# Performance work log

Hardware: AMD Instinct MI355X
Metric: run time of the kernel (lower is better)

## Reference

```python
import jax, jax.numpy as jnp
import numpy as np

B, S, D = 8, 2048, 512
FF = 2048
E = 8

def setup_inputs() -> dict:
    key = jax.random.key(0)
    ks = jax.random.split(key, 7)
    s = 1.0 / np.sqrt(D)
    sf = 1.0 / np.sqrt(FF)
    return {
        "x":  jax.random.normal(ks[0], (B, S, D), dtype=jnp.float32),
        "Wg": jax.random.uniform(ks[1], (D, E), jnp.float32, -s, s),
        "bg": jax.random.uniform(ks[2], (E,), jnp.float32, -s, s),
        "W1": jax.random.uniform(ks[3], (E, D, FF), jnp.float32, -s, s),
        "b1": jax.random.uniform(ks[4], (E, FF), jnp.float32, -s, s),
        "W2": jax.random.uniform(ks[5], (E, FF, D), jnp.float32, -sf, sf),
        "b2": jax.random.uniform(ks[6], (E, D), jnp.float32, -sf, sf),
    }

def reference(x, Wg, bg, W1, b1, W2, b2):
    b, s, d = x.shape
    xf = x.reshape(-1, d)                      # [T, D]
    logits = xf @ Wg + bg                      # [T, E]
    probs = jax.nn.softmax(logits, axis=-1)
    pmax = jnp.max(probs, axis=-1)             # [T]
    routes = jnp.argmax(probs, axis=-1)        # [T] int
    xs = xf * pmax[:, None]                    # scale tokens by router prob
    # per-expert FFN over all tokens, select the routed expert's output
    out_tok = jnp.zeros_like(xf)
    for e in range(E):
        h = jax.nn.relu(xs @ W1[e] + b1[e])    # [T, FF]
        y = h @ W2[e] + b2[e]                  # [T, D]
        out_tok = jnp.where((routes == e)[:, None], y, out_tok)
    # torch.cat of per-expert nonzero-index gathers == tokens stably sorted by expert id
    order = jnp.argsort(routes)                # jnp.argsort is stable
    return out_tok[order].reshape(b, s, d)
```

## Files before the change

### kernel.cpp

```cpp
#include <hip/hip_runtime.h>
#include <hip/hip_bf16.h>

constexpr int TTOK  = 16384;
constexpr int DDIM  = 512;
constexpr int FFDIM = 2048;
constexpr int NEXP  = 8;
constexpr int GB_TOK = 16;
constexpr int NGB    = TTOK / GB_TOK;
constexpr int MAXTILES = TTOK / 128 + NEXP;
constexpr int TRW1_BLOCKS = 4096;
constexpr int TRW2_XBLK   = 256;

typedef __attribute__((ext_vector_type(8))) short short8_t;
typedef __attribute__((ext_vector_type(4))) float f32x4_t;

__device__ __forceinline__ unsigned short f2bf(float f) {
    union { float f; unsigned u; } v; v.f = f;
    return (unsigned short)((v.u + 0x7fffu + ((v.u >> 16) & 1u)) >> 16);
}

__device__ __forceinline__ void gl_lds16(const void* g, void* l) {
    __builtin_amdgcn_global_load_lds(
        (const __attribute__((address_space(1))) void*)g,
        (__attribute__((address_space(3))) void*)l,
        16, 0, 0);
}

__device__ __forceinline__ void tr_tile(const float* __restrict__ src,
                                        unsigned short* __restrict__ dst,
                                        int R, int C, int tileId, float* lds) {
    int tilesC = C / 32;
    int c0 = (tileId % tilesC) * 32;
    int r0 = (tileId / tilesC) * 64;
    int t = threadIdx.x;
    int lr = t >> 3;
    int ls = t & 7;
    #pragma unroll
    for (int rb = 0; rb < 2; rb++) {
        int row = rb * 32 + lr;
        float4 v = *(const float4*)(src + (size_t)(r0 + row) * C + c0 + 4 * ls);
        int p4 = (4 * ls) ^ (8 * ((row >> 3) & 3));
        *(float4*)(lds + row * 36 + p4) = v;
    }
    __syncthreads();
    int c = t >> 3;
    int b = t & 7;
    union { short8_t v; unsigned short s[8]; } o;
    #pragma unroll
    for (int j = 0; j < 8; j++) {
        int r = 8 * b + j;
        int p = c ^ (8 * ((r >> 3) & 3));
        o.s[j] = f2bf(lds[r * 36 + p]);
    }
    *(short8_t*)(dst + (size_t)(c0 + c) * R + r0 + 8 * b) = o.v;
}

__global__ __launch_bounds__(256) void gate_kernel(const float* __restrict__ x,
                                                   const float* __restrict__ Wg,
                                                   const float* __restrict__ bg,
                                                   int* __restrict__ route,
                                                   float* __restrict__ pmax,
                                                   int* __restrict__ blockCounts) {
    int tid = threadIdx.x;
    __shared__ int cnt[NEXP];
    __shared__ float bgs[NEXP];
    int gb = blockIdx.x;
    if (tid < NEXP) { cnt[tid] = 0; bgs[tid] = bg[tid]; }
    __syncthreads();
    int wave = tid >> 6, lane = tid & 63;
    float w[8][8];
    #pragma unroll
    for (int jj = 0; jj < 8; jj++) {
        float4 a = *(const float4*)(Wg + (size_t)(lane * 8 + jj) * NEXP);
        float4 b = *(const float4*)(Wg + (size_t)(lane * 8 + jj) * NEXP + 4);
        w[jj][0] = a.x; w[jj][1] = a.y; w[jj][2] = a.z; w[jj][3] = a.w;
        w[jj][4] = b.x; w[jj][5] = b.y; w[jj][6] = b.z; w[jj][7] = b.w;
    }
    int tbase = gb * GB_TOK + wave * 4;
    for (int it = 0; it < 4; it++) {
        int t = tbase + it;
        float4 xa = *(const float4*)(x + (size_t)t * DDIM + lane * 8);
        float4 xb = *(const float4*)(x + (size_t)t * DDIM + lane * 8 + 4);
        float xs[8] = {xa.x, xa.y, xa.z, xa.w, xb.x, xb.y, xb.z, xb.w};
        double acc[NEXP];
        #pragma unroll
        for (int e = 0; e < NEXP; e++) acc[e] = 0.0;
        #pragma unroll
        for (int jj = 0; jj < 8; jj++) {
            double xv = (double)xs[jj];
            #pragma unroll
            for (int e = 0; e < NEXP; e++) acc[e] += xv * (double)w[jj][e];
        }
        #pragma unroll
        for (int off = 32; off > 0; off >>= 1) {
            #pragma unroll
            for (int e = 0; e < NEXP; e++) acc[e] += __shfl_down(acc[e], off);
        }
        if (lane == 0) {
            double l[NEXP];
            #pragma unroll
            for (int e = 0; e < NEXP; e++) l[e] = acc[e] + (double)bgs[e];
            int r = 0; double lm = l[0];
            #pragma unroll
            for (int e = 1; e < NEXP; e++) if (l[e] > lm) { lm = l[e]; r = e; }
            float s = 0.0f;
            #pragma unroll
            for (int e = 0; e < NEXP; e++) s += __expf((float)(l[e] - lm));
            route[t] = r;
            pmax[t] = 1.0f / s;
            atomicAdd(&cnt[r], 1);
        }
    }
    __syncthreads();
    if (tid < NEXP) blockCounts[gb * NEXP + tid] = cnt[tid];
}

__global__ __launch_bounds__(256) void scatter_kernel(const float* __restrict__ x,
                                                      const int* __restrict__ route,
                                                      const float* __restrict__ pmax,
                                                      const int* __restrict__ blockCounts,
                                                      unsigned short* __restrict__ Xs,
                                                      int* __restrict__ segPrefix,
                                                      int* __restrict__ tilePrefix,
                                                      const float* __restrict__ W1,
                                                      unsigned short* __restrict__ W1T) {
    int tid = threadIdx.x;
    if (blockIdx.x >= NGB) {
        __shared__ __align__(16) float tlds[64 * 36];
        int id = blockIdx.x - NGB;
        int e = id >> 9;
        int tile = id & 511;
        tr_tile(W1 + (size_t)e * DDIM * FFDIM, W1T + (size_t)e * DDIM * FFDIM,
                DDIM, FFDIM, tile, tlds);
        return;
    }
    int bb = blockIdx.x;
    int wave = tid >> 6, lane = tid & 63;

    int tot[NEXP], pre[NEXP];
    #pragma unroll
    for (int e = 0; e < NEXP; e++) { tot[e] = 0; pre[e] = 0; }
    for (int b = tid; b < NGB; b += 256) {
        #pragma unroll
        for (int e = 0; e < NEXP; e++) {
            int c = blockCounts[b * NEXP + e];
            tot[e] += c;
            if (b < bb) pre[e] += c;
        }
    }
    #pragma unroll
    for (int off = 32; off > 0; off >>= 1) {
        #pragma unroll
        for (int e = 0; e < NEXP; e++) {
            tot[e] += __shfl_down(tot[e], off);
            pre[e] += __shfl_down(pre[e], off);
        }
    }
    __shared__ int stot[4][NEXP], spre[4][NEXP];
    __shared__ int boff[NEXP];
    if (lane == 0) {
        #pragma unroll
        for (int e = 0; e < NEXP; e++) { stot[wave][e] = tot[e]; spre[wave][e] = pre[e]; }
    }
    __syncthreads();
    if (tid == 0) {
        int T[NEXP], P[NEXP];
        #pragma unroll
        for (int e = 0; e < NEXP; e++) {
            T[e] = stot[0][e] + stot[1][e] + stot[2][e] + stot[3][e];
            P[e] = spre[0][e] + spre[1][e] + spre[2][e] + spre[3][e];
        }
        int s = 0;
        #pragma unroll
        for (int e = 0; e < NEXP; e++) { boff[e] = s + P[e]; s += T[e]; }
        if (bb == 0) {
            int ss = 0, tp = 0;
            segPrefix[0] = 0; tilePrefix[0] = 0;
            #pragma unroll
            for (int e = 0; e < NEXP; e++) {
                ss += T[e]; tp += (T[e] + 127) >> 7;
                segPrefix[e + 1] = ss; tilePrefix[e + 1] = tp;
            }
        }
    }
    __syncthreads();

    __shared__ int dstL[GB_TOK];
    __shared__ float pmL[GB_TOK];
    if (tid < GB_TOK) {
        int t = bb * GB_TOK + tid;
        int r = route[t];
        unsigned long long ltmask = (tid == 0) ? 0ull : ((~0ull) >> (64 - tid));
        int rank = 0;
        #pragma unroll
        for (int e = 0; e < NEXP; e++) {
            unsigned long long m = __ballot(r == e);
            if (r == e) rank = __popcll(m & ltmask);
        }
        dstL[tid] = boff[r] + rank;
        pmL[tid] = pmax[t];
    }
    __syncthreads();
    for (int rr = 0; rr < 4; rr++) {
        int rowl = wave * 4 + rr;
        int t = bb * GB_TOK + rowl;
        float pm = pmL[rowl];
        const float4* xr = (const float4*)(x + (size_t)t * DDIM) + lane * 2;
        float4 a = xr[0], b = xr[1];
        union { short8_t v; unsigned short s[8]; } o;
        o.s[0] = f2bf(a.x * pm); o.s[1] = f2bf(a.y * pm);
        o.s[2] = f2bf(a.z * pm); o.s[3] = f2bf(a.w * pm);
        o.s[4] = f2bf(b.x * pm); o.s[5] = f2bf(b.y * pm);
        o.s[6] = f2bf(b.z * pm); o.s[7] = f2bf(b.w * pm);
        *(short8_t*)(Xs + (size_t)dstL[rowl] * DDIM + lane * 8) = o.v;
    }
}

__global__ __launch_bounds__(256) void gemm1_fused(const unsigned short* __restrict__ A,
                                                   const unsigned short* __restrict__ Bt,
                                                   const float* __restrict__ bias,
                                                   unsigned short* __restrict__ C,
                                                   const int* __restrict__ segPrefix,
                                                   const int* __restrict__ tilePrefix,
                                                   const float* __restrict__ W2,
                                                   unsigned short* __restrict__ W2T) {
    constexpr int K = DDIM, N = FFDIM;
    __shared__ __align__(16) unsigned short SMEM[16384];

    if (blockIdx.x >= MAXTILES) {
        int id = (blockIdx.x - MAXTILES) * 16 + blockIdx.y;
        int e = id >> 9;
        int tile = id & 511;
        tr_tile(W2 + (size_t)e * DDIM * FFDIM, W2T + (size_t)e * DDIM * FFDIM,
                FFDIM, DDIM, tile, (float*)SMEM);
        return;
    }

    int bx = blockIdx.x;
    bx = (bx & 7) * (MAXTILES / 8) + (bx >> 3);
    int t = bx;
    if (t >= tilePrefix[NEXP]) return;
    int e = 0;
    #pragma unroll
    for (int i = 1; i <= NEXP; i++) e += (t >= tilePrefix[i]) ? 1 : 0;
    int seg1 = segPrefix[e + 1];
    int m0 = segPrefix[e] + (t - tilePrefix[e]) * 128;
    int n0 = blockIdx.y * 128;

    unsigned short* As = SMEM;
    unsigned short* Bs = SMEM + 8192;

    int tid = threadIdx.x, wave = tid >> 6, lane = tid & 63;
    const unsigned short* Bte = Bt + (size_t)e * N * K;

    int srow = lane >> 2;
    int sg   = (lane & 3) ^ ((lane >> 2) & 3) ^ ((lane >> 4) & 3);
    int scol = sg * 8;

    f32x4_t acc[4][4];
    #pragma unroll
    for (int i = 0; i < 4; i++)
        #pragma unroll
        for (int j = 0; j < 4; j++) acc[i][j] = (f32x4_t){0.f, 0.f, 0.f, 0.f};

    int wm = (wave & 1) * 64;
    int wn = (wave >> 1) * 64;
    int frow = lane & 15;
    int gr = lane >> 4;
    int fswz = (gr ^ (frow & 3) ^ ((frow >> 2) & 3)) * 8;

    int reg0 = wave * 2;
    int arow0 = m0 + reg0 * 16 + srow;
    arow0 = arow0 < TTOK ? arow0 : TTOK - 1;
    int arow1 = m0 + (reg0 + 1) * 16 + srow;
    arow1 = arow1 < TTOK ? arow1 : TTOK - 1;
    const unsigned short* aptr0 = A + (size_t)arow0 * K + scol;
    const unsigned short* aptr1 = A + (size_t)arow1 * K + scol;
    const unsigned short* bptr0 = Bte + (size_t)(n0 + reg0 * 16 + srow) * K + scol;
    const unsigned short* bptr1 = Bte + (size_t)(n0 + (reg0 + 1) * 16 + srow) * K + scol;

    #pragma unroll
    for (int kc = 0; kc < K; kc += 64) {
        #pragma unroll
        for (int p = 0; p < 2; p++) {
            gl_lds16(aptr0 + kc + p * 32, &As[p * 4096 + reg0 * 512]);
            gl_lds16(aptr1 + kc + p * 32, &As[p * 4096 + (reg0 + 1) * 512]);
            gl_lds16(bptr0 + kc + p * 32, &Bs[p * 4096 + reg0 * 512]);
            gl_lds16(bptr1 + kc + p * 32, &Bs[p * 4096 + (reg0 + 1) * 512]);
        }
        __syncthreads();
        #pragma unroll
        for (int p = 0; p < 2; p++) {
            short8_t af[4], bfr[4];
            #pragma unroll
            for (int i = 0; i < 4; i++)
                af[i] = *(const short8_t*)&As[p * 4096 + (wm + i * 16 + frow) * 32 + fswz];
            #pragma unroll
            for (int j = 0; j < 4; j++)
                bfr[j] = *(const short8_t*)&Bs[p * 4096 + (wn + j * 16 + frow) * 32 + fswz];
            #pragma unroll
            for (int i = 0; i < 4; i++)
                #pragma unroll
                for (int j = 0; j < 4; j++)
                    acc[i][j] = __builtin_amdgcn_mfma_f32_16x16x32_bf16(af[i], bfr[j], acc[i][j], 0, 0, 0);
        }
        __syncthreads();
    }

    int quad = lane >> 4;
    int colb = lane & 15;
    float bv[4];
    #pragma unroll
    for (int j = 0; j < 4; j++) bv[j] = bias[(size_t)e * N + n0 + wn + j * 16 + colb];

    unsigned short* cbuf = As;
    #pragma unroll
    for (int p = 0; p < 2; p++) {
        __syncthreads();
        if ((wave >> 1) == p) {
            #pragma unroll
            for (int i = 0; i < 4; i++)
                #pragma unroll
                for (int j = 0; j < 4; j++)
                    #pragma unroll
                    for (int r = 0; r < 4; r++) {
                        float v = acc[i][j][r] + bv[j];
                        v = fmaxf(v, 0.0f);
                        int wrow = wm + i * 16 + quad * 4 + r;
                        int cc = (j * 16 + colb) ^ (((wrow >> 3) & 1) * 16);
                        cbuf[wrow * 72 + cc] = f2bf(v);
                    }
        }
        __syncthreads();
        int row = tid >> 1, ch = (tid & 1) * 32;
        int grow = m0 + row;
        if (grow < seg1) {
            #pragma unroll
            for (int k = 0; k < 4; k++) {
                int vv = (ch + k * 8) ^ (((row >> 3) & 1) * 16);
                short8_t v = *(const short8_t*)&cbuf[row * 72 + vv];
                *(short8_t*)&C[(size_t)grow * N + n0 + p * 64 + ch + k * 8] = v;
            }
        }
    }
}

template <bool RELU, typename OutT, int K, int N>
__global__ __launch_bounds__(256) void gemm_seg(const unsigned short* __restrict__ A,
                                                const unsigned short* __restrict__ Bt,
                                                const float* __restrict__ bias,
                                                OutT* __restrict__ C,
                                                const int* __restrict__ segPrefix,
                                                const int* __restrict__ tilePrefix) {
    int bx = blockIdx.x;
    bx = (bx & 7) * (MAXTILES / 8) + (bx >> 3);
    int t = bx;
    if (t >= tilePrefix[NEXP]) return;
    int e = 0;
    #pragma unroll
    for (int i = 1; i <= NEXP; i++) e += (t >= tilePrefix[i]) ? 1 : 0;
    int seg1 = segPrefix[e + 1];
    int m0 = segPrefix[e] + (t - tilePrefix[e]) * 128;
    int n0 = blockIdx.y * 128;

    __shared__ unsigned short As[2 * 4096];
    __shared__ unsigned short Bs[2 * 4096];

    int tid = threadIdx.x, wave = tid >> 6, lane = tid & 63;
    const unsigned short* Bte = Bt + (size_t)e * N * K;

    int srow = lane >> 2;
    int sg   = (lane & 3) ^ ((lane >> 2) & 3) ^ ((lane >> 4) & 3);
    int scol = sg * 8;

    f32x4_t acc[4][4];
    #pragma unroll
    for (int i = 0; i < 4; i++)
        #pragma unroll
        for (int j = 0; j < 4; j++) acc[i][j] = (f32x4_t){0.f, 0.f, 0.f, 0.f};

    int wm = (wave & 1) * 64;
    int wn = (wave >> 1) * 64;
    int frow = lane & 15;
    int gr = lane >> 4;
    int fswz = (gr ^ (frow & 3) ^ ((frow >> 2) & 3)) * 8;

    int reg0 = wave * 2;
    int arow0 = m0 + reg0 * 16 + srow;
    arow0 = arow0 < TTOK ? arow0 : TTOK - 1;
    int arow1 = m0 + (reg0 + 1) * 16 + srow;
    arow1 = arow1 < TTOK ? arow1 : TTOK - 1;
    const unsigned short* aptr0 = A + (size_t)arow0 * K + scol;
    const unsigned short* aptr1 = A + (size_t)arow1 * K + scol;
    const unsigned short* bptr0 = Bte + (size_t)(n0 + reg0 * 16 + srow) * K + scol;
    const unsigned short* bptr1 = Bte + (size_t)(n0 + (reg0 + 1) * 16 + srow) * K + scol;

    #pragma unroll
    for (int kc = 0; kc < K; kc += 64) {
        #pragma unroll
        for (int p = 0; p < 2; p++) {
            gl_lds16(aptr0 + kc + p * 32, &As[p * 4096 + reg0 * 512]);
            gl_lds16(aptr1 + kc + p * 32, &As[p * 4096 + (reg0 + 1) * 512]);
            gl_lds16(bptr0 + kc + p * 32, &Bs[p * 4096 + reg0 * 512]);
            gl_lds16(bptr1 + kc + p * 32, &Bs[p * 4096 + (reg0 + 1) * 512]);
        }
        __syncthreads();
        #pragma unroll
        for (int p = 0; p < 2; p++) {
            short8_t af[4], bfr[4];
            #pragma unroll
            for (int i = 0; i < 4; i++)
                af[i] = *(const short8_t*)&As[p * 4096 + (wm + i * 16 + frow) * 32 + fswz];
            #pragma unroll
            for (int j = 0; j < 4; j++)
                bfr[j] = *(const short8_t*)&Bs[p * 4096 + (wn + j * 16 + frow) * 32 + fswz];
            #pragma unroll
            for (int i = 0; i < 4; i++)
                #pragma unroll
                for (int j = 0; j < 4; j++)
                    acc[i][j] = __builtin_amdgcn_mfma_f32_16x16x32_bf16(af[i], bfr[j], acc[i][j], 0, 0, 0);
        }
        __syncthreads();
    }

    int quad = lane >> 4;
    int colb = lane & 15;
    float bv[4];
    #pragma unroll
    for (int j = 0; j < 4; j++) bv[j] = bias[(size_t)e * N + n0 + wn + j * 16 + colb];

    #pragma unroll
    for (int i = 0; i < 4; i++) {
        #pragma unroll
        for (int j = 0; j < 4; j++) {
            int col = n0 + wn + j * 16 + colb;
            #pragma unroll
            for (int r = 0; r < 4; r++) {
                int row = m0 + wm + i * 16 + quad * 4 + r;
                if (row < seg1) {
                    float v = acc[i][j][r] + bv[j];
                    if (RELU) v = fmaxf(v, 0.0f);
                    C[(size_t)row * N + col] = v;
                }
            }
        }
    }
}

extern "C" void kernel_launch(void* const* d_in, const int* in_sizes, int n_in,
                              void* d_out, int out_size, void* d_ws, size_t ws_size,
                              hipStream_t stream) {
    const float* x  = (const float*)d_in[0];
    const float* Wg = (const float*)d_in[1];
    const float* bg = (const float*)d_in[2];
    const float* W1 = (const float*)d_in[3];
    const float* b1 = (const float*)d_in[4];
    const float* W2 = (const float*)d_in[5];
    const float* b2 = (const float*)d_in[6];
    float* out = (float*)d_out;

    char* ws = (char*)d_ws;
    size_t off = 0;
    auto alloc = [&](size_t bytes) -> char* {
        char* p = ws + off;
        off += (bytes + 255) & ~(size_t)255;
        return p;
    };
    unsigned short* W1T = (unsigned short*)alloc((size_t)NEXP * DDIM * FFDIM * 2);
    unsigned short* W2T = (unsigned short*)alloc((size_t)NEXP * DDIM * FFDIM * 2);
    unsigned short* Xs  = (unsigned short*)alloc((size_t)TTOK * DDIM * 2);
    unsigned short* H   = (unsigned short*)alloc((size_t)TTOK * FFDIM * 2);
    int*   route        = (int*)alloc((size_t)TTOK * 4);
    float* pmaxArr      = (float*)alloc((size_t)TTOK * 4);
    int*   blockCounts  = (int*)alloc((size_t)NGB * NEXP * 4);
    int*   segPrefix    = (int*)alloc((size_t)(NEXP + 1) * 4);
    int*   tilePrefix   = (int*)alloc((size_t)(NEXP + 1) * 4);

    gate_kernel<<<NGB, 256, 0, stream>>>(x, Wg, bg, route, pmaxArr, blockCounts);
    scatter_kernel<<<NGB + TRW1_BLOCKS, 256, 0, stream>>>(
        x, route, pmaxArr, blockCounts, Xs, segPrefix, tilePrefix, W1, W1T);
    gemm1_fused<<<dim3(MAXTILES + TRW2_XBLK, FFDIM / 128, 1), 256, 0, stream>>>(
        Xs, W1T, b1, H, segPrefix, tilePrefix, W2, W2T);
    gemm_seg<false, float, FFDIM, DDIM><<<dim3(MAXTILES, DDIM / 128, 1), 256, 0, stream>>>(
        H, W2T, b2, out, segPrefix, tilePrefix);
}
```

Baseline: 286.2 us.

## Fuse gate and scatter kernels with a grid-wide atomic barrier

Merges the gating kernel into the scatter/W1-transpose kernel. Routes and pmax now stay in shared memory instead of round-tripping through global arrays, and a spin-wait on a global atomic counter replaces the kernel boundary. This drops one launch and the route/pmax traffic. It relies on all 1024 gate blocks being co-resident, since otherwise the spin barrier can deadlock; launch_bounds(256,4) is set to help with that. It also adds a memset launch for the counter.

```diff
diff --git a/kernel.cpp b/kernel.cpp
--- a/kernel.cpp
+++ b/kernel.cpp
@@ -55,75 +55,17 @@
     *(short8_t*)(dst + (size_t)(c0 + c) * R + r0 + 8 * b) = o.v;
 }
 
-__global__ __launch_bounds__(256) void gate_kernel(const float* __restrict__ x,
-                                                   const float* __restrict__ Wg,
-                                                   const float* __restrict__ bg,
-                                                   int* __restrict__ route,
-                                                   float* __restrict__ pmax,
-                                                   int* __restrict__ blockCounts) {
-    int tid = threadIdx.x;
-    __shared__ int cnt[NEXP];
-    __shared__ float bgs[NEXP];
-    int gb = blockIdx.x;
-    if (tid < NEXP) { cnt[tid] = 0; bgs[tid] = bg[tid]; }
-    __syncthreads();
-    int wave = tid >> 6, lane = tid & 63;
-    float w[8][8];
-    #pragma unroll
-    for (int jj = 0; jj < 8; jj++) {
-        float4 a = *(const float4*)(Wg + (size_t)(lane * 8 + jj) * NEXP);
-        float4 b = *(const float4*)(Wg + (size_t)(lane * 8 + jj) * NEXP + 4);
-        w[jj][0] = a.x; w[jj][1] = a.y; w[jj][2] = a.z; w[jj][3] = a.w;
-        w[jj][4] = b.x; w[jj][5] = b.y; w[jj][6] = b.z; w[jj][7] = b.w;
-    }
-    int tbase = gb * GB_TOK + wave * 4;
-    for (int it = 0; it < 4; it++) {
-        int t = tbase + it;
-        float4 xa = *(const float4*)(x + (size_t)t * DDIM + lane * 8);
-        float4 xb = *(const float4*)(x + (size_t)t * DDIM + lane * 8 + 4);
-        float xs[8] = {xa.x, xa.y, xa.z, xa.w, xb.x, xb.y, xb.z, xb.w};
-        double acc[NEXP];
-        #pragma unroll
-        for (int e = 0; e < NEXP; e++) acc[e] = 0.0;
-        #pragma unroll
-        for (int jj = 0; jj < 8; jj++) {
-            double xv = (double)xs[jj];
-            #pragma unroll
-            for (int e = 0; e < NEXP; e++) acc[e] += xv * (double)w[jj][e];
-        }
-        #pragma unroll
-        for (int off = 32; off > 0; off >>= 1) {
-            #pragma unroll
-            for (int e = 0; e < NEXP; e++) acc[e] += __shfl_down(acc[e], off);
-        }
-        if (lane == 0) {
-            double l[NEXP];
-            #pragma unroll
-            for (int e = 0; e < NEXP; e++) l[e] = acc[e] + (double)bgs[e];
-            int r = 0; double lm = l[0];
-            #pragma unroll
-            for (int e = 1; e < NEXP; e++) if (l[e] > lm) { lm = l[e]; r = e; }
-            float s = 0.0f;
-            #pragma unroll
-            for (int e = 0; e < NEXP; e++) s += __expf((float)(l[e] - lm));
-            route[t] = r;
-            pmax[t] = 1.0f / s;
-            atomicAdd(&cnt[r], 1);
-        }
-    }
-    __syncthreads();
-    if (tid < NEXP) blockCounts[gb * NEXP + tid] = cnt[tid];
-}
-
-__global__ __launch_bounds__(256) void scatter_kernel(const float* __restrict__ x,
-                                                      const int* __restrict__ route,
-                                                      const float* __restrict__ pmax,
-                                                      const int* __restrict__ blockCounts,
-                                                      unsigned short* __restrict__ Xs,
-                                                      int* __restrict__ segPrefix,
-                                                      int* __restrict__ tilePrefix,
-                                                      const float* __restrict__ W1,
-                                                      unsigned short* __restrict__ W1T) {
+__global__ __launch_bounds__(256, 4) void gate_scatter(
+        const float* __restrict__ x,
+        const float* __restrict__ Wg,
+        const float* __restrict__ bg,
+        int* __restrict__ blockCounts,
+        unsigned int* __restrict__ counter,
+        unsigned short* __restrict__ Xs,
+        int* __restrict__ segPrefix,
+        int* __restrict__ tilePrefix,
+        const float* __restrict__ W1,
+        unsigned short* __restrict__ W1T) {
     int tid = threadIdx.x;
     if (blockIdx.x >= NGB) {
         __shared__ __align__(16) float tlds[64 * 36];
@@ -134,8 +76,72 @@
                 DDIM, FFDIM, tile, tlds);
         return;
     }
-    int bb = blockIdx.x;
+
+    __shared__ int cnt[NEXP];
+    __shared__ float bgs[NEXP];
+    __shared__ int rtL[GB_TOK];
+    __shared__ float pmL[GB_TOK];
+    int gb = blockIdx.x;
+    if (tid < NEXP) { cnt[tid] = 0; bgs[tid] = bg[tid]; }
+    __syncthreads();
     int wave = tid >> 6, lane = tid & 63;
+
+    {
+        float w[8][8];
+        #pragma unroll
+        for (int jj = 0; jj < 8; jj++) {
+            float4 a = *(const float4*)(Wg + (size_t)(lane * 8 + jj) * NEXP);
+            float4 b = *(const float4*)(Wg + (size_t)(lane * 8 + jj) * NEXP + 4);
+            w[jj][0] = a.x; w[jj][1] = a.y; w[jj][2] = a.z; w[jj][3] = a.w;
+            w[jj][4] = b.x; w[jj][5] = b.y; w[jj][6] = b.z; w[jj][7] = b.w;
+        }
+        int tbase = gb * GB_TOK + wave * 4;
+        for (int it = 0; it < 4; it++) {
+            int t = tbase + it;
+            float4 xa = *(const float4*)(x + (size_t)t * DDIM + lane * 8);
+            float4 xb = *(const float4*)(x + (size_t)t * DDIM + lane * 8 + 4);
+            float xs[8] = {xa.x, xa.y, xa.z, xa.w, xb.x, xb.y, xb.z, xb.w};
+            double acc[NEXP];
+            #pragma unroll
+            for (int e = 0; e < NEXP; e++) acc[e] = 0.0;
+            #pragma unroll
+            for (int jj = 0; jj < 8; jj++) {
+                double xv = (double)xs[jj];
+                #pragma unroll
+                for (int e = 0; e < NEXP; e++) acc[e] += xv * (double)w[jj][e];
+            }
+            #pragma unroll
+            for (int off = 32; off > 0; off >>= 1) {
+                #pragma unroll
+                for (int e = 0; e < NEXP; e++) acc[e] += __shfl_down(acc[e], off);
+            }
+            if (lane == 0) {
+                double l[NEXP];
+                #pragma unroll
+                for (int e = 0; e < NEXP; e++) l[e] = acc[e] + (double)bgs[e];
+                int r = 0; double lm = l[0];
+                #pragma unroll
+                for (int e = 1; e < NEXP; e++) if (l[e] > lm) { lm = l[e]; r = e; }
+                float s = 0.0f;
+                #pragma unroll
+                for (int e = 0; e < NEXP; e++) s += __expf((float)(l[e] - lm));
+                rtL[wave * 4 + it] = r;
+                pmL[wave * 4 + it] = 1.0f / s;
+                atomicAdd(&cnt[r], 1);
+            }
+        }
+    }
+    __syncthreads();
+    if (tid < NEXP) blockCounts[gb * NEXP + tid] = cnt[tid];
+    __syncthreads();
+
+    if (tid == 0) {
+        __threadfence();
+        atomicAdd(counter, 1u);
+        while (__hip_atomic_load(counter, __ATOMIC_ACQUIRE, __HIP_MEMORY_SCOPE_AGENT) < (unsigned)NGB)
+            __builtin_amdgcn_s_sleep(8);
+    }
+    __syncthreads();
 
     int tot[NEXP], pre[NEXP];
     #pragma unroll
@@ -143,9 +149,10 @@
     for (int b = tid; b < NGB; b += 256) {
         #pragma unroll
         for (int e = 0; e < NEXP; e++) {
-            int c = blockCounts[b * NEXP + e];
+            int c = __hip_atomic_load(&blockCounts[b * NEXP + e],
+                                      __ATOMIC_RELAXED, __HIP_MEMORY_SCOPE_AGENT);
             tot[e] += c;
-            if (b < bb) pre[e] += c;
+            if (b < gb) pre[e] += c;
         }
     }
     #pragma unroll
@@ -173,7 +180,7 @@
         int s = 0;
         #pragma unroll
         for (int e = 0; e < NEXP; e++) { boff[e] = s + P[e]; s += T[e]; }
-        if (bb == 0) {
+        if (gb == 0) {
             int ss = 0, tp = 0;
             segPrefix[0] = 0; tilePrefix[0] = 0;
             #pragma unroll
@@ -186,10 +193,8 @@
     __syncthreads();
 
     __shared__ int dstL[GB_TOK];
-    __shared__ float pmL[GB_TOK];
     if (tid < GB_TOK) {
-        int t = bb * GB_TOK + tid;
-        int r = route[t];
+        int r = rtL[tid];
         unsigned long long ltmask = (tid == 0) ? 0ull : ((~0ull) >> (64 - tid));
         int rank = 0;
         #pragma unroll
@@ -198,12 +203,11 @@
             if (r == e) rank = __popcll(m & ltmask);
         }
         dstL[tid] = boff[r] + rank;
-        pmL[tid] = pmax[t];
     }
     __syncthreads();
     for (int rr = 0; rr < 4; rr++) {
         int rowl = wave * 4 + rr;
-        int t = bb * GB_TOK + rowl;
+        int t = gb * GB_TOK + rowl;
         float pm = pmL[rowl];
         const float4* xr = (const float4*)(x + (size_t)t * DDIM) + lane * 2;
         float4 a = xr[0], b = xr[1];
@@ -470,15 +474,14 @@
     unsigned short* W2T = (unsigned short*)alloc((size_t)NEXP * DDIM * FFDIM * 2);
     unsigned short* Xs  = (unsigned short*)alloc((size_t)TTOK * DDIM * 2);
     unsigned short* H   = (unsigned short*)alloc((size_t)TTOK * FFDIM * 2);
-    int*   route        = (int*)alloc((size_t)TTOK * 4);
-    float* pmaxArr      = (float*)alloc((size_t)TTOK * 4);
     int*   blockCounts  = (int*)alloc((size_t)NGB * NEXP * 4);
     int*   segPrefix    = (int*)alloc((size_t)(NEXP + 1) * 4);
     int*   tilePrefix   = (int*)alloc((size_t)(NEXP + 1) * 4);
-
-    gate_kernel<<<NGB, 256, 0, stream>>>(x, Wg, bg, route, pmaxArr, blockCounts);
-    scatter_kernel<<<NGB + TRW1_BLOCKS, 256, 0, stream>>>(
-        x, route, pmaxArr, blockCounts, Xs, segPrefix, tilePrefix, W1, W1T);
+    unsigned int* counter = (unsigned int*)alloc(256);
+
+    hipMemsetAsync(counter, 0, sizeof(unsigned int), stream);
+    gate_scatter<<<NGB + TRW1_BLOCKS, 256, 0, stream>>>(
+        x, Wg, bg, blockCounts, counter, Xs, segPrefix, tilePrefix, W1, W1T);
     gemm1_fused<<<dim3(MAXTILES + TRW2_XBLK, FFDIM / 128, 1), 256, 0, stream>>>(
         Xs, W1T, b1, H, segPrefix, tilePrefix, W2, W2T);
     gemm_seg<false, float, FFDIM, DDIM><<<dim3(MAXTILES, DDIM / 128, 1), 256, 0, stream>>>(
```

Measured after the change: 534.8 us. 86.8% more time.
